# Optimization experiments

Hardware: AMD Instinct MI355X
Metric: run time of the kernel (lower is better)

Reference implementation:

```python
import jax, jax.numpy as jnp
import numpy as np

B, S, D, H, E, K = 4, 2048, 1024, 4096, 8, 2
CAP_RATIO = 1.05


def setup_inputs() -> dict:
    key = jax.random.key(0)
    k0, k1, k2, k3 = jax.random.split(key, 4)
    x = jax.random.normal(k0, (B, S, D), jnp.float32)
    # router gating weight (xavier-uniform-ish scale)
    Wg = jax.random.normal(k1, (E, D), jnp.float32) * np.float32(np.sqrt(2.0 / (D + E)))
    W1 = jax.random.normal(k2, (E, D, H), jnp.float32) * np.float32(0.02)
    b1 = jnp.zeros((E, H), jnp.float32)
    W2 = jax.random.normal(k3, (E, H, D), jnp.float32) * np.float32(0.02)
    b2 = jnp.zeros((E, D), jnp.float32)
    return {"x": x, "Wg": Wg, "W1": W1, "b1": b1, "W2": W2, "b2": b2}


def reference(x, Wg, W1, b1, W2, b2):
    Bs, Ss, Dd = x.shape
    T = Bs * Ss
    C = int(round(K * T * CAP_RATIO / E))  # static buffer capacity per expert
    xf = x.reshape(T, Dd)

    # --- router (eval mode: no noise) ---
    logits = xf @ Wg.T                       # (T, E)
    gates = jax.nn.softmax(logits, axis=-1)  # (T, E)
    topv, topi = jax.lax.top_k(gates, K)     # (T, K)

    # --- capacity-limited dispatch: FCFS over slot-major (slot, token) order ---
    idx_sm = topi.T.reshape(-1)                              # (K*T,) slot-major expert ids
    oh = jax.nn.one_hot(idx_sm, E, dtype=jnp.int32)          # (K*T, E)
    pos_sm = (jnp.cumsum(oh, axis=0) * oh).sum(-1) - 1       # 0-based rank within expert
    within_sm = pos_sm < C
    pos_sm = jnp.where(within_sm, pos_sm, C)                 # C == out-of-bounds sentinel
    pos = pos_sm.reshape(K, T).T                             # (T, K)
    within = within_sm.reshape(K, T).T                       # (T, K) bool

    # --- combine weights: mask dropped slots, renormalize over active slots ---
    w = topv * within.astype(topv.dtype)
    sums = w.sum(-1, keepdims=True)
    w = jnp.where(sums > 0, w / sums, w)

    # --- scatter tokens into per-expert capacity buffers ---
    e_flat = topi.reshape(-1)                                # (T*K,)
    pos_flat = pos.reshape(-1)                               # (T*K,)
    x_ts = jnp.broadcast_to(xf[:, None, :], (T, K, Dd)).reshape(T * K, Dd)
    expert_in = jnp.zeros((E, C, Dd), x.dtype).at[e_flat, pos_flat].set(x_ts, mode='drop')

    # --- per-expert MLP (grouped GEMM) ---
    h = jax.nn.gelu(jnp.einsum('ecd,edh->ech', expert_in, W1) + b1[:, None, :], approximate=False)
    o = jnp.einsum('ech,ehd->ecd', h, W2) + b2[:, None, :]   # (E, C, D)

    # --- gather back and weighted combine (dropped slots gather 0) ---
    y_ts = o.at[e_flat, pos_flat].get(mode='fill', fill_value=0).reshape(T, K, Dd)
    y = jnp.einsum('tk,tkd->td', w, y_ts)                    # (T, D)

    # --- auxiliary losses ---
    imp = gates.sum(0)                                       # (E,)
    l_imp = (jnp.std(imp) / (imp.mean() + 1e-6)) ** 2
    tpe = (oh * within_sm[:, None].astype(jnp.int32)).sum(0).astype(jnp.float32)
    l_load = (jnp.std(tpe) / (tpe.mean() + 1e-6)) ** 2
    l_aux = 0.5 * (l_imp + l_load)

    return y.reshape(Bs, Ss, Dd), l_aux, l_load
```

## Files before the change

kernel.cpp:

```cpp
#include <hip/hip_runtime.h>
#include <math.h>

typedef short short8v __attribute__((ext_vector_type(8)));
typedef float f32x4 __attribute__((ext_vector_type(4)));
typedef unsigned short ushort4v __attribute__((ext_vector_type(4)));

#define T_TOK 8192
#define DDIM 1024
#define HDIM 4096
#define NE 8
#define CCAP 2150
#define CPAD 2304

__device__ __forceinline__ unsigned short f2bf(float f) {
  union { float f; unsigned u; } a; a.f = f;
  unsigned r = a.u + 0x7fffu + ((a.u >> 16) & 1u);
  return (unsigned short)(r >> 16);
}
__device__ __forceinline__ float bf2f(unsigned short h) {
  union { unsigned u; float f; } a; a.u = ((unsigned)h) << 16;
  return a.f;
}

#define GLOAD_LDS16(gp, lp)                                                   \
  __builtin_amdgcn_global_load_lds(                                           \
      (const __attribute__((address_space(1))) void*)(gp),                    \
      (__attribute__((address_space(3))) void*)(lp), 16, 0, 0)

__device__ __forceinline__ short8v ds_read128(unsigned addr) {
  short8v v;
  asm volatile("ds_read_b128 %0, %1" : "=v"(v) : "v"(addr));
  return v;
}

#define BAR() __builtin_amdgcn_s_barrier()

__global__ __launch_bounds__(256) void router_kernel(
    const float* __restrict__ x, const float* __restrict__ Wg,
    int2* __restrict__ topi, float2* __restrict__ topv,
    float* __restrict__ blkimp) {
  __shared__ float wg[NE * DDIM];
  __shared__ float gsh[4][NE];
  int tid = threadIdx.x;
  for (int i = tid; i < NE * DDIM / 4; i += 256)
    ((float4*)wg)[i] = ((const float4*)Wg)[i];
  __syncthreads();
  int w = tid >> 6, lane = tid & 63;
  int t = blockIdx.x * 4 + w;
  const float* xr = x + (size_t)t * DDIM;
  float p[NE] = {0.f, 0.f, 0.f, 0.f, 0.f, 0.f, 0.f, 0.f};
#pragma unroll
  for (int j = 0; j < 16; ++j) {
    float xv = xr[lane + 64 * j];
#pragma unroll
    for (int e = 0; e < NE; ++e)
      p[e] = fmaf(xv, wg[e * DDIM + lane + 64 * j], p[e]);
  }
#pragma unroll
  for (int e = 0; e < NE; ++e) {
#pragma unroll
    for (int off = 32; off > 0; off >>= 1) p[e] += __shfl_xor(p[e], off, 64);
  }
  float mx = p[0];
#pragma unroll
  for (int e = 1; e < NE; ++e) mx = fmaxf(mx, p[e]);
  float g[NE];
  float s = 0.f;
#pragma unroll
  for (int e = 0; e < NE; ++e) { g[e] = expf(p[e] - mx); s += g[e]; }
  float inv = 1.0f / s;
#pragma unroll
  for (int e = 0; e < NE; ++e) g[e] *= inv;
  int i0 = 0; float v0 = g[0];
#pragma unroll
  for (int e = 1; e < NE; ++e) if (g[e] > v0) { v0 = g[e]; i0 = e; }
  int i1 = -1; float v1 = -1.0f;
#pragma unroll
  for (int e = 0; e < NE; ++e)
    if (e != i0 && g[e] > v1) { v1 = g[e]; i1 = e; }
  if (lane == 0) {
    topi[t] = make_int2(i0, i1);
    topv[t] = make_float2(v0, v1);
#pragma unroll
    for (int e = 0; e < NE; ++e) gsh[w][e] = g[e];
  }
  __syncthreads();
  if (tid < NE)
    blkimp[blockIdx.x * NE + tid] =
        gsh[0][tid] + gsh[1][tid] + gsh[2][tid] + gsh[3][tid];
}

__global__ __launch_bounds__(256) void dispatch_kernel(
    const int2* __restrict__ topi, const float2* __restrict__ topv,
    const float* __restrict__ blkimp, int2* __restrict__ posmj,
    float2* __restrict__ wmaj, float* __restrict__ tail) {
  __shared__ unsigned char eid[2 * T_TOK];
  __shared__ unsigned short possm[2 * T_TOK];
  __shared__ int cnt_sh[NE];
  __shared__ float part[32][NE];
  int tid = threadIdx.x;
  for (int i = tid; i < T_TOK; i += 256) {
    int2 ti = topi[i];
    eid[i] = (unsigned char)ti.x;
    eid[T_TOK + i] = (unsigned char)ti.y;
  }
  __syncthreads();
  if (tid < 64) {
    int lane = tid;
    unsigned long long low = (1ull << lane) - 1ull;
    int c0 = 0, c1 = 0, c2 = 0, c3 = 0, c4 = 0, c5 = 0, c6 = 0, c7 = 0;
    for (int base = 0; base < 2 * T_TOK; base += 64) {
      int e = eid[base + lane];
      unsigned long long m0 = __ballot(e == 0);
      unsigned long long m1 = __ballot(e == 1);
      unsigned long long m2 = __ballot(e == 2);
      unsigned long long m3 = __ballot(e == 3);
      unsigned long long m4 = __ballot(e == 4);
      unsigned long long m5 = __ballot(e == 5);
      unsigned long long m6 = __ballot(e == 6);
      unsigned long long m7 = __ballot(e == 7);
      int rank = 0;
      if (e == 0) rank = c0 + __popcll(m0 & low);
      if (e == 1) rank = c1 + __popcll(m1 & low);
      if (e == 2) rank = c2 + __popcll(m2 & low);
      if (e == 3) rank = c3 + __popcll(m3 & low);
      if (e == 4) rank = c4 + __popcll(m4 & low);
      if (e == 5) rank = c5 + __popcll(m5 & low);
      if (e == 6) rank = c6 + __popcll(m6 & low);
      if (e == 7) rank = c7 + __popcll(m7 & low);
      possm[base + lane] = (unsigned short)((rank < CCAP) ? rank : CCAP);
      c0 += __popcll(m0); c1 += __popcll(m1); c2 += __popcll(m2);
      c3 += __popcll(m3); c4 += __popcll(m4); c5 += __popcll(m5);
      c6 += __popcll(m6); c7 += __popcll(m7);
    }
    if (lane == 0) {
      cnt_sh[0] = c0; cnt_sh[1] = c1; cnt_sh[2] = c2; cnt_sh[3] = c3;
      cnt_sh[4] = c4; cnt_sh[5] = c5; cnt_sh[6] = c6; cnt_sh[7] = c7;
    }
  }
  __syncthreads();
  for (int t = tid; t < T_TOK; t += 256) {
    int p0 = possm[t], p1 = possm[T_TOK + t];
    float2 tv = topv[t];
    float w0 = (p0 < CCAP) ? tv.x : 0.0f;
    float w1 = (p1 < CCAP) ? tv.y : 0.0f;
    float s = w0 + w1;
    if (s > 0.0f) { w0 /= s; w1 /= s; }
    posmj[t] = make_int2(p0, p1);
    wmaj[t] = make_float2(w0, w1);
  }
  {
    int sl = tid >> 3, e8 = tid & 7;
    float s = 0.f;
    for (int b = sl; b < 2048; b += 32) s += blkimp[b * NE + e8];
    part[sl][e8] = s;
  }
  __syncthreads();
  if (tid == 0) {
    float imp[NE], te[NE];
    for (int e = 0; e < NE; ++e) {
      float s = 0.f;
      for (int j = 0; j < 32; ++j) s += part[j][e];
      imp[e] = s;
      int c = cnt_sh[e];
      te[e] = (float)(c < CCAP ? c : CCAP);
    }
    float mi = 0.f, mt = 0.f;
    for (int e = 0; e < NE; ++e) { mi += imp[e]; mt += te[e]; }
    mi *= 0.125f; mt *= 0.125f;
    float vi = 0.f, vt = 0.f;
    for (int e = 0; e < NE; ++e) {
      vi += (imp[e] - mi) * (imp[e] - mi);
      vt += (te[e] - mt) * (te[e] - mt);
    }
    vi *= 0.125f; vt *= 0.125f;
    float ai = sqrtf(vi) / (mi + 1e-6f);
    float at = sqrtf(vt) / (mt + 1e-6f);
    tail[0] = 0.5f * (ai * ai + at * at);
    tail[1] = at * at;
  }
}

__global__ __launch_bounds__(256) void scatter_kernel(
    const float* __restrict__ x, const int2* __restrict__ topi,
    const int2* __restrict__ posmj, unsigned short* __restrict__ ein) {
  int tid = threadIdx.x;
  int gid = blockIdx.x * 4 + (tid >> 6);
  int lane = tid & 63;
  int t = gid >> 1, k = gid & 1;
  int2 pp = posmj[t];
  int p = k ? pp.y : pp.x;
  if (p >= CCAP) return;
  int2 ii = topi[t];
  int e = k ? ii.y : ii.x;
  const float4* src = (const float4*)(x + (size_t)t * DDIM);
  unsigned short* dst = ein + ((size_t)e * CPAD + p) * DDIM;
#pragma unroll
  for (int j = 0; j < 4; ++j) {
    int c = j * 64 + lane;
    float4 v = src[c];
    ushort4v o;
    o.x = f2bf(v.x); o.y = f2bf(v.y); o.z = f2bf(v.z); o.w = f2bf(v.w);
    *(ushort4v*)(dst + (size_t)c * 4) = o;
  }
}

__global__ __launch_bounds__(256) void transpose_cvt_kernel(
    const float* __restrict__ W, unsigned short* __restrict__ WT, int R,
    int Cc) {
  __shared__ unsigned short tile[64][72];
  int rt = R >> 6, ct = Cc >> 6;
  int per_e = rt * ct;
  int e = blockIdx.x / per_e;
  int rem = blockIdx.x % per_e;
  int tr = rem % rt, tc = rem / rt;
  int r0 = tr << 6, c0 = tc << 6;
  const float* We = W + (size_t)e * R * Cc;
  unsigned short* WTe = WT + (size_t)e * R * Cc;
  int tid = threadIdx.x;
  {
    int rl = tid >> 2, cb = (tid & 3) << 4;
    const float* src = We + (size_t)(r0 + rl) * Cc + c0 + cb;
#pragma unroll
    for (int j = 0; j < 16; j += 4) {
      float4 v = *(const float4*)(src + j);
      tile[rl][cb + j + 0] = f2bf(v.x);
      tile[rl][cb + j + 1] = f2bf(v.y);
      tile[rl][cb + j + 2] = f2bf(v.z);
      tile[rl][cb + j + 3] = f2bf(v.w);
    }
  }
  __syncthreads();
  {
    int cl = tid >> 2, rb = (tid & 3) << 4;
    unsigned short* dst = WTe + (size_t)(c0 + cl) * R + r0 + rb;
#pragma unroll
    for (int j = 0; j < 16; j += 4) {
      ushort4v o;
      o.x = tile[rb + j + 0][cl];
      o.y = tile[rb + j + 1][cl];
      o.z = tile[rb + j + 2][cl];
      o.w = tile[rb + j + 3][cl];
      *(ushort4v*)(dst + j) = o;
    }
  }
}

template <bool GELU>
__global__ __launch_bounds__(512, 2) void gemm256_kernel(
    const unsigned short* __restrict__ A, const unsigned short* __restrict__ B,
    const float* __restrict__ bias, unsigned short* __restrict__ Out0,
    unsigned short* __restrict__ Out1, int M, int N, int Kz, int Ksub, int NT,
    int mt, int nt) {
  __shared__ __align__(16) char smem[131072];
  int nwg = gridDim.x;
  int bid = blockIdx.x;
  int swz = (bid & 7) * (nwg >> 3) + (bid >> 3);
  int bm = swz % mt;
  int r = swz / mt;
  int bn = r % nt;
  int r2 = r / nt;
  int e = r2 & 7;
  int ks = r2 >> 3;
  unsigned short* Outp = ks ? Out1 : Out0;
  int koff = ks * Ksub;

  int tid = threadIdx.x;
  int w = tid >> 6, lane = tid & 63;
  int wm = w >> 2, wn = w & 3;
  int fr = lane & 15, g = lane >> 4;
  size_t Kzs = (size_t)Kz;
  const char* Ab = (const char*)(A + ((size_t)e * M + (size_t)bm * 256) * Kzs + koff);
  const char* Bb = (const char*)(B + ((size_t)e * N + (size_t)bn * 256) * Kzs + koff);

  size_t ro0 = (size_t)(w * 16 + fr) * Kzs * 2 + (size_t)g * 16;
  size_t ro1 = ro0 + (size_t)128 * Kzs * 2;
  int ld0 = (w << 10) + lane * 16;
  int ld1 = ((8 + w) << 10) + lane * 16;

  auto stage = [&](const char* gb, int buf, int isB, int kh) {
    int base = (isB << 16) + (buf << 15) + (kh << 14);
    GLOAD_LDS16(gb + ro0 + kh * 64, smem + base + ld0);
    GLOAD_LDS16(gb + ro1 + kh * 64, smem + base + ld1);
  };

  unsigned sbase =
      (unsigned)(unsigned long long)(__attribute__((address_space(3))) char*)smem;
  unsigned l16 = (unsigned)(lane * 16);
  unsigned am = sbase + (unsigned)((wm * 8) << 10) + l16;
  unsigned bnr = sbase + 65536u + (unsigned)((wn * 4) << 10) + l16;

  f32x4 acc[8][4] = {};
  short8v Af0[8], Af1[8], Bk0[4], Bk1[4];

#define MM32(AF, BK)                                                       \
  do {                                                                     \
    __builtin_amdgcn_s_setprio(1);                                         \
    _Pragma("unroll") for (int m_ = 0; m_ < 8; ++m_)                       \
        _Pragma("unroll") for (int n_ = 0; n_ < 4; ++n_)                   \
            acc[m_][n_] = __builtin_amdgcn_mfma_f32_16x16x32_bf16(         \
                AF[m_], BK[n_], acc[m_][n_], 0, 0, 0);                     \
    __builtin_amdgcn_s_setprio(0);                                         \
    __builtin_amdgcn_sched_barrier(0);                                     \
  } while (0)

  stage(Ab, 0, 0, 0); stage(Ab, 0, 0, 1);
  stage(Bb, 0, 1, 0); stage(Bb, 0, 1, 1);
  asm volatile("s_waitcnt vmcnt(0)");
  BAR();

  for (int t = 0; t < NT; ++t) {
    int c = t & 1, cn = c ^ 1;
    unsigned cb = (unsigned)(c << 15);
    if (t + 1 < NT) {
      const char* At1 = Ab + (size_t)(t + 1) * 128;
      const char* Bt1 = Bb + (size_t)(t + 1) * 128;
      stage(At1, cn, 0, 0); stage(At1, cn, 0, 1);
      stage(Bt1, cn, 1, 0); stage(Bt1, cn, 1, 1);
    }
#pragma unroll
    for (int n = 0; n < 4; ++n) Bk0[n] = ds_read128(bnr + cb + (n << 10));
#pragma unroll
    for (int m = 0; m < 8; ++m) Af0[m] = ds_read128(am + cb + (m << 10));
#pragma unroll
    for (int n = 0; n < 4; ++n)
      Bk1[n] = ds_read128(bnr + cb + 16384u + (n << 10));
#pragma unroll
    for (int m = 0; m < 8; ++m)
      Af1[m] = ds_read128(am + cb + 16384u + (m << 10));
    asm volatile("s_waitcnt lgkmcnt(12)");
    __builtin_amdgcn_sched_barrier(0);
    MM32(Af0, Bk0);
    asm volatile("s_waitcnt lgkmcnt(0)");
    __builtin_amdgcn_sched_barrier(0);
    MM32(Af1, Bk1);
    asm volatile("s_waitcnt vmcnt(0)");
    BAR();
  }
#undef MM32

  float bv[4];
#pragma unroll
  for (int n = 0; n < 4; ++n)
    bv[n] = (ks == 0)
                ? bias[(size_t)e * N + (size_t)bn * 256 + wn * 64 + n * 16 + fr]
                : 0.0f;
  char* wreg = smem + w * 16384;
#pragma unroll
  for (int m = 0; m < 8; ++m)
#pragma unroll
    for (int n = 0; n < 4; ++n)
#pragma unroll
      for (int j = 0; j < 4; ++j) {
        float v = acc[m][n][j] + bv[n];
        if (GELU) v = 0.5f * v * (1.0f + erff(v * 0.70710678118654752f));
        int rl = m * 16 + g * 4 + j;
        *(unsigned short*)(wreg + rl * 128 + (n * 16 + fr) * 2) = f2bf(v);
      }
  unsigned short* Oe = Outp +
                       ((size_t)e * M + (size_t)bm * 256 + (size_t)wm * 128) * N +
                       (size_t)bn * 256 + (size_t)wn * 64;
#pragma unroll
  for (int pass = 0; pass < 16; ++pass) {
    int rr = pass * 8 + (lane >> 3);
    int ch = lane & 7;
    short8v vv = *(const short8v*)(wreg + rr * 128 + ch * 16);
    *(short8v*)(Oe + (size_t)rr * N + ch * 8) = vv;
  }
}

__global__ __launch_bounds__(256) void gather_kernel(
    const unsigned short* __restrict__ obufA,
    const unsigned short* __restrict__ obufB, const int2* __restrict__ topi,
    const int2* __restrict__ posmj, const float2* __restrict__ wmaj,
    float* __restrict__ y) {
  int tid = threadIdx.x;
  int w = tid >> 6, lane = tid & 63;
  int t = blockIdx.x * 4 + w;
  int2 pp = posmj[t];
  int2 ii = topi[t];
  float2 ww = wmaj[t];
  float* yr = y + (size_t)t * DDIM;
  size_t o0 = ((size_t)ii.x * CPAD + pp.x) * DDIM;
  size_t o1 = ((size_t)ii.y * CPAD + pp.y) * DDIM;
  bool v0 = pp.x < CCAP, v1 = pp.y < CCAP;
#pragma unroll
  for (int j = 0; j < 4; ++j) {
    int c = j * 64 + lane;
    float ax = 0.f, ay = 0.f, az = 0.f, aw = 0.f;
    if (v0) {
      ushort4v a = *(const ushort4v*)(obufA + o0 + (size_t)c * 4);
      ushort4v b = *(const ushort4v*)(obufB + o0 + (size_t)c * 4);
      ax += ww.x * (bf2f(a.x) + bf2f(b.x));
      ay += ww.x * (bf2f(a.y) + bf2f(b.y));
      az += ww.x * (bf2f(a.z) + bf2f(b.z));
      aw += ww.x * (bf2f(a.w) + bf2f(b.w));
    }
    if (v1) {
      ushort4v a = *(const ushort4v*)(obufA + o1 + (size_t)c * 4);
      ushort4v b = *(const ushort4v*)(obufB + o1 + (size_t)c * 4);
      ax += ww.y * (bf2f(a.x) + bf2f(b.x));
      ay += ww.y * (bf2f(a.y) + bf2f(b.y));
      az += ww.y * (bf2f(a.z) + bf2f(b.z));
      aw += ww.y * (bf2f(a.w) + bf2f(b.w));
    }
    ((float4*)yr)[c] = make_float4(ax, ay, az, aw);
  }
}

extern "C" void kernel_launch(void* const* d_in, const int* in_sizes, int n_in,
                              void* d_out, int out_size, void* d_ws,
                              size_t ws_size, hipStream_t stream) {
  (void)in_sizes; (void)n_in; (void)out_size; (void)ws_size;
  const float* x = (const float*)d_in[0];
  const float* Wg = (const float*)d_in[1];
  const float* W1 = (const float*)d_in[2];
  const float* b1 = (const float*)d_in[3];
  const float* W2 = (const float*)d_in[4];
  const float* b2 = (const float*)d_in[5];
  float* out = (float*)d_out;

  char* ws = (char*)d_ws;
  size_t off = 0;
  auto alloc = [&](size_t b) {
    char* p = ws + off;
    off += (b + 255) & ~(size_t)255;
    return p;
  };
  unsigned short* ein = (unsigned short*)alloc((size_t)NE * CPAD * DDIM * 2);
  unsigned short* hbuf = (unsigned short*)alloc((size_t)NE * CPAD * HDIM * 2);
  unsigned short* obuf = (unsigned short*)alloc((size_t)NE * CPAD * DDIM * 2);
  unsigned short* w1t = (unsigned short*)alloc((size_t)NE * HDIM * DDIM * 2);
  unsigned short* w2t = (unsigned short*)alloc((size_t)NE * DDIM * HDIM * 2);
  int2* topi = (int2*)alloc(T_TOK * sizeof(int2));
  float2* topv = (float2*)alloc(T_TOK * sizeof(float2));
  int2* posmj = (int2*)alloc(T_TOK * sizeof(int2));
  float2* wmaj = (float2*)alloc(T_TOK * sizeof(float2));
  float* blkimp = (float*)alloc(2048 * NE * sizeof(float));

  transpose_cvt_kernel<<<NE * (DDIM / 64) * (HDIM / 64), 256, 0, stream>>>(
      W1, w1t, DDIM, HDIM);
  transpose_cvt_kernel<<<NE * (HDIM / 64) * (DDIM / 64), 256, 0, stream>>>(
      W2, w2t, HDIM, DDIM);
  router_kernel<<<T_TOK / 4, 256, 0, stream>>>(x, Wg, topi, topv, blkimp);
  dispatch_kernel<<<1, 256, 0, stream>>>(topi, topv, blkimp, posmj, wmaj,
                                         out + (size_t)T_TOK * DDIM);
  scatter_kernel<<<(2 * T_TOK) / 4, 256, 0, stream>>>(x, topi, posmj, ein);

  gemm256_kernel<true><<<NE * 9 * 16, 512, 0, stream>>>(
      ein, w1t, b1, hbuf, hbuf, CPAD, HDIM, DDIM, DDIM, DDIM / 64, 9, 16);
  gemm256_kernel<false><<<NE * 9 * 4 * 2, 512, 0, stream>>>(
      hbuf, w2t, b2, obuf, ein, CPAD, DDIM, HDIM, HDIM / 2, HDIM / 128, 9, 4);

  gather_kernel<<<T_TOK / 4, 256, 0, stream>>>(obuf, ein, topi, posmj, wmaj,
                                               out);
}
```

Measured before the change: 728.2 us.

## Replace direct global-to-LDS loads with register-staged prefetch pipeline in GEMM

The grouped GEMM kernel stops using global_load_lds direct-to-shared copies with hand-placed waitcnt, setprio and sched_barrier control. It now loads the next-next K tile into registers, computes on the current shared buffer, then writes the staged registers into the other buffer before a __syncthreads. This hides global latency through a register prefetch stage and leaves instruction scheduling to the compiler. In exchange it uses more VGPRs and extra LDS write instructions, and it loses the manual MFMA priority and scheduling hints.

```diff
diff --git a/kernel.cpp b/kernel.cpp
--- a/kernel.cpp
+++ b/kernel.cpp
@@ -21,19 +21,6 @@
   union { unsigned u; float f; } a; a.u = ((unsigned)h) << 16;
   return a.f;
 }
-
-#define GLOAD_LDS16(gp, lp)                                                   \
-  __builtin_amdgcn_global_load_lds(                                           \
-      (const __attribute__((address_space(1))) void*)(gp),                    \
-      (__attribute__((address_space(3))) void*)(lp), 16, 0, 0)
-
-__device__ __forceinline__ short8v ds_read128(unsigned addr) {
-  short8v v;
-  asm volatile("ds_read_b128 %0, %1" : "=v"(v) : "v"(addr));
-  return v;
-}
-
-#define BAR() __builtin_amdgcn_s_barrier()
 
 __global__ __launch_bounds__(256) void router_kernel(
     const float* __restrict__ x, const float* __restrict__ Wg,
@@ -247,7 +234,7 @@
 }
 
 template <bool GELU>
-__global__ __launch_bounds__(512, 2) void gemm256_kernel(
+__global__ __launch_bounds__(512, 2) void gemm256_rs(
     const unsigned short* __restrict__ A, const unsigned short* __restrict__ B,
     const float* __restrict__ bias, unsigned short* __restrict__ Out0,
     unsigned short* __restrict__ Out1, int M, int N, int Kz, int Ksub, int NT,
@@ -278,66 +265,65 @@
   int ld0 = (w << 10) + lane * 16;
   int ld1 = ((8 + w) << 10) + lane * 16;
 
-  auto stage = [&](const char* gb, int buf, int isB, int kh) {
-    int base = (isB << 16) + (buf << 15) + (kh << 14);
-    GLOAD_LDS16(gb + ro0 + kh * 64, smem + base + ld0);
-    GLOAD_LDS16(gb + ro1 + kh * 64, smem + base + ld1);
+  short8v st[8];
+  auto gload = [&](const char* a, const char* b) {
+    st[0] = *(const short8v*)(a + ro0);
+    st[1] = *(const short8v*)(a + ro1);
+    st[2] = *(const short8v*)(a + ro0 + 64);
+    st[3] = *(const short8v*)(a + ro1 + 64);
+    st[4] = *(const short8v*)(b + ro0);
+    st[5] = *(const short8v*)(b + ro1);
+    st[6] = *(const short8v*)(b + ro0 + 64);
+    st[7] = *(const short8v*)(b + ro1 + 64);
   };
-
-  unsigned sbase =
-      (unsigned)(unsigned long long)(__attribute__((address_space(3))) char*)smem;
-  unsigned l16 = (unsigned)(lane * 16);
-  unsigned am = sbase + (unsigned)((wm * 8) << 10) + l16;
-  unsigned bnr = sbase + 65536u + (unsigned)((wn * 4) << 10) + l16;
+  auto swrite = [&](int buf) {
+    char* p = smem + (buf << 15);
+    *(short8v*)(p + ld0) = st[0];
+    *(short8v*)(p + ld1) = st[1];
+    *(short8v*)(p + 16384 + ld0) = st[2];
+    *(short8v*)(p + 16384 + ld1) = st[3];
+    *(short8v*)(p + 65536 + ld0) = st[4];
+    *(short8v*)(p + 65536 + ld1) = st[5];
+    *(short8v*)(p + 65536 + 16384 + ld0) = st[6];
+    *(short8v*)(p + 65536 + 16384 + ld1) = st[7];
+  };
+  auto lda = [&](int buf, int kk, int m16) -> short8v {
+    return *(const short8v*)(smem + (buf << 15) + (kk << 14) + (m16 << 10) +
+                             lane * 16);
+  };
+  auto ldb = [&](int buf, int kk, int n16) -> short8v {
+    return *(const short8v*)(smem + 65536 + (buf << 15) + (kk << 14) +
+                             (n16 << 10) + lane * 16);
+  };
 
   f32x4 acc[8][4] = {};
-  short8v Af0[8], Af1[8], Bk0[4], Bk1[4];
-
-#define MM32(AF, BK)                                                       \
-  do {                                                                     \
-    __builtin_amdgcn_s_setprio(1);                                         \
-    _Pragma("unroll") for (int m_ = 0; m_ < 8; ++m_)                       \
-        _Pragma("unroll") for (int n_ = 0; n_ < 4; ++n_)                   \
-            acc[m_][n_] = __builtin_amdgcn_mfma_f32_16x16x32_bf16(         \
-                AF[m_], BK[n_], acc[m_][n_], 0, 0, 0);                     \
-    __builtin_amdgcn_s_setprio(0);                                         \
-    __builtin_amdgcn_sched_barrier(0);                                     \
-  } while (0)
-
-  stage(Ab, 0, 0, 0); stage(Ab, 0, 0, 1);
-  stage(Bb, 0, 1, 0); stage(Bb, 0, 1, 1);
-  asm volatile("s_waitcnt vmcnt(0)");
-  BAR();
+
+  gload(Ab, Bb);
+  swrite(0);
+  gload(Ab + 128, Bb + 128);
+  __syncthreads();
 
   for (int t = 0; t < NT; ++t) {
-    int c = t & 1, cn = c ^ 1;
-    unsigned cb = (unsigned)(c << 15);
-    if (t + 1 < NT) {
-      const char* At1 = Ab + (size_t)(t + 1) * 128;
-      const char* Bt1 = Bb + (size_t)(t + 1) * 128;
-      stage(At1, cn, 0, 0); stage(At1, cn, 0, 1);
-      stage(Bt1, cn, 1, 0); stage(Bt1, cn, 1, 1);
-    }
-#pragma unroll
-    for (int n = 0; n < 4; ++n) Bk0[n] = ds_read128(bnr + cb + (n << 10));
-#pragma unroll
-    for (int m = 0; m < 8; ++m) Af0[m] = ds_read128(am + cb + (m << 10));
-#pragma unroll
-    for (int n = 0; n < 4; ++n)
-      Bk1[n] = ds_read128(bnr + cb + 16384u + (n << 10));
-#pragma unroll
-    for (int m = 0; m < 8; ++m)
-      Af1[m] = ds_read128(am + cb + 16384u + (m << 10));
-    asm volatile("s_waitcnt lgkmcnt(12)");
-    __builtin_amdgcn_sched_barrier(0);
-    MM32(Af0, Bk0);
-    asm volatile("s_waitcnt lgkmcnt(0)");
-    __builtin_amdgcn_sched_barrier(0);
-    MM32(Af1, Bk1);
-    asm volatile("s_waitcnt vmcnt(0)");
-    BAR();
-  }
-#undef MM32
+    int c = t & 1;
+#pragma unroll
+    for (int kk = 0; kk < 2; ++kk) {
+      short8v bv4[4], av;
+#pragma unroll
+      for (int n = 0; n < 4; ++n) bv4[n] = ldb(c, kk, wn * 4 + n);
+#pragma unroll
+      for (int m = 0; m < 8; ++m) {
+        av = lda(c, kk, wm * 8 + m);
+#pragma unroll
+        for (int n = 0; n < 4; ++n)
+          acc[m][n] = __builtin_amdgcn_mfma_f32_16x16x32_bf16(av, bv4[n],
+                                                              acc[m][n], 0, 0, 0);
+      }
+    }
+    if (t + 1 < NT) swrite(c ^ 1);
+    if (t + 2 < NT)
+      gload(Ab + (size_t)(t + 2) * 128, Bb + (size_t)(t + 2) * 128);
+    __syncthreads();
+  }
 
   float bv[4];
 #pragma unroll
@@ -447,9 +433,9 @@
                                          out + (size_t)T_TOK * DDIM);
   scatter_kernel<<<(2 * T_TOK) / 4, 256, 0, stream>>>(x, topi, posmj, ein);
 
-  gemm256_kernel<true><<<NE * 9 * 16, 512, 0, stream>>>(
+  gemm256_rs<true><<<NE * 9 * 16, 512, 0, stream>>>(
       ein, w1t, b1, hbuf, hbuf, CPAD, HDIM, DDIM, DDIM, DDIM / 64, 9, 16);
-  gemm256_kernel<false><<<NE * 9 * 4 * 2, 512, 0, stream>>>(
+  gemm256_rs<false><<<NE * 9 * 4 * 2, 512, 0, stream>>>(
       hbuf, w2t, b2, obuf, ein, CPAD, DDIM, HDIM, HDIM / 2, HDIM / 128, 9, 4);
 
   gather_kernel<<<T_TOK / 4, 256, 0, stream>>>(obuf, ein, topi, posmj, wmaj,
```

After: 665.8 us, median of 3. 1.09x faster.
